# Performance work log

Measured on AMD Instinct MI355X. Metric: run time of the kernel, lower is better.

Reference implementation:

```python
import jax, jax.numpy as jnp
import numpy as np

B, S = 4, 2048          # batch, seq tokens
D_IN, D_HID = 1280, 2048  # from CAMERAMOE emb_size / d_inner
E, K = 8, 2             # num_experts, top_k
LN_EPS = 1e-6


def setup_inputs() -> dict:
    key = jax.random.key(0)
    ks = jax.random.split(key, 8)
    rn = lambda k, shp, sc=1.0: jax.random.normal(k, shp, dtype=jnp.float32) * sc
    return {
        "x": rn(ks[0], (B, S, D_IN)),
        "noise": rn(ks[1], (B, S, E)),          # the randn_like draw, made explicit
        "wr": rn(ks[2], (D_IN, E), 0.02), "br": jnp.zeros((E,), jnp.float32),
        "wn": rn(ks[3], (D_IN, E), 0.02), "bn": jnp.zeros((E,), jnp.float32),
        "w1": rn(ks[4], (E, D_IN, D_HID), 0.02), "b1": jnp.zeros((E, D_HID), jnp.float32),
        "w2": rn(ks[5], (E, D_HID, D_IN), 0.02), "b2": jnp.zeros((E, D_IN), jnp.float32),
        "gamma": jnp.ones((E, D_IN), jnp.float32), "beta": jnp.zeros((E, D_IN), jnp.float32),
    }


def reference(x, noise, wr, br, wn, bn, w1, b1, w2, b2, gamma, beta):
    # --- NoisyTopkRouter ---
    logits = x @ wr + br                                  # [B,S,E]
    noise_logits = x @ wn + bn                            # [B,S,E]
    noisy = logits + noise * jax.nn.softplus(noise_logits)
    _, idx = jax.lax.top_k(noisy, K)                      # [B,S,K]
    sel = jax.nn.one_hot(idx, E, dtype=bool).any(axis=-2) # [B,S,E] selected-expert mask
    sparse_logits = jnp.where(sel, noisy, -jnp.inf)       # scatter of top-k logits into -inf
    gates = jax.nn.softmax(sparse_logits, axis=-1)        # zeros for non-selected experts

    # --- SparseMoE combine (gate-weighted sum over experts; gate==0 masks out
    # non-selected tokens, matching the torch masked gather/scatter-add math) ---
    h = jax.nn.relu(jnp.einsum('bsd,edh->ebsh', x, w1) + b1[:, None, None, :])
    y = jnp.einsum('ebsh,ehd->ebsd', h, w2) + b2[:, None, None, :]
    y = y + x                                             # residual (broadcast over E)
    mu = y.mean(axis=-1, keepdims=True)
    var = y.var(axis=-1, keepdims=True)
    y = (y - mu) * jax.lax.rsqrt(var + LN_EPS)
    y = y * gamma[:, None, None, :] + beta[:, None, None, :]
    return jnp.einsum('ebsd,bse->bsd', y, gates)          # [B,S,D_IN]
```

## Files before the change

### kernel.cpp

```cpp
#include <hip/hip_runtime.h>
#include <stdint.h>

typedef unsigned short u16;
typedef __attribute__((ext_vector_type(8))) short short8;
typedef __attribute__((ext_vector_type(4))) float f32x4;
typedef __attribute__((ext_vector_type(4))) float float4v;
typedef __attribute__((ext_vector_type(4))) unsigned short us4;
typedef __attribute__((ext_vector_type(8))) unsigned short us8;

#define TOK   8192
#define DIN   1280
#define DHID  2048
#define NEXP  8
#define RCAP  17408
#define MT128 136

#define TRBLK1 5120
#define TRBLK2 5120
#define GABLKS 2048

__device__ __forceinline__ float bf2f(u16 u) {
  union { unsigned int i; float f; } v; v.i = ((unsigned int)u) << 16; return v.f;
}
__device__ __forceinline__ u16 f2bf(float f) {
  union { float f; unsigned int i; } v; v.f = f;
  unsigned int x = v.i;
  return (u16)((x + 0x7fffu + ((x >> 16) & 1u)) >> 16);
}

__device__ __forceinline__ void gload16(const u16* g, void* lds) {
  __builtin_amdgcn_global_load_lds(
      (const __attribute__((address_space(1))) unsigned int*)g,
      (__attribute__((address_space(3))) unsigned int*)lds, 16, 0, 0);
}

__global__ __launch_bounds__(256) void router_k(
    const float* __restrict__ x, const float* __restrict__ noise,
    const float* __restrict__ wr, const float* __restrict__ br,
    const float* __restrict__ wn, const float* __restrict__ bn,
    int* __restrict__ topk_e, float* __restrict__ topk_g)
{
  int w = threadIdx.x >> 6, lane = threadIdx.x & 63;
  int t0 = blockIdx.x * 8 + w * 2;
  int h = lane & 1, dl = lane >> 1;
  const float* xA = x + (size_t)t0 * DIN;
  const float* xB = xA + DIN;

  float ra[4], na[4], rb2[4], nb2[4];
  #pragma unroll
  for (int j = 0; j < 4; j++) { ra[j] = 0.f; na[j] = 0.f; rb2[j] = 0.f; nb2[j] = 0.f; }

  #pragma unroll 4
  for (int d0 = 0; d0 < DIN; d0 += 32) {
    int d = d0 + dl;
    float4v wrv = *(const float4v*)(wr + (size_t)d * 8 + h * 4);
    float4v wnv = *(const float4v*)(wn + (size_t)d * 8 + h * 4);
    float xa = xA[d], xb = xB[d];
    #pragma unroll
    for (int j = 0; j < 4; j++) {
      ra[j]  += xa * wrv[j]; na[j]  += xa * wnv[j];
      rb2[j] += xb * wrv[j]; nb2[j] += xb * wnv[j];
    }
  }
  #pragma unroll
  for (int off = 2; off < 64; off <<= 1) {
    #pragma unroll
    for (int j = 0; j < 4; j++) {
      ra[j]  += __shfl_xor(ra[j],  off);
      na[j]  += __shfl_xor(na[j],  off);
      rb2[j] += __shfl_xor(rb2[j], off);
      nb2[j] += __shfl_xor(nb2[j], off);
    }
  }
  float raO[4], naO[4], rbO[4], nbO[4];
  #pragma unroll
  for (int j = 0; j < 4; j++) {
    raO[j] = __shfl_xor(ra[j], 1);
    naO[j] = __shfl_xor(na[j], 1);
    rbO[j] = __shfl_xor(rb2[j], 1);
    nbO[j] = __shfl_xor(nb2[j], 1);
  }
  if (lane == 0) {
    #pragma unroll
    for (int tt = 0; tt < 2; tt++) {
      int t = t0 + tt;
      float noisy[8];
      #pragma unroll
      for (int j = 0; j < 4; j++) {
        float lg0 = (tt ? rb2[j] : ra[j]) + br[j];
        float nl0 = (tt ? nb2[j] : na[j]) + bn[j];
        float lg1 = (tt ? rbO[j] : raO[j]) + br[4 + j];
        float nl1 = (tt ? nbO[j] : naO[j]) + bn[4 + j];
        float sp0 = (nl0 > 0.f) ? nl0 + log1pf(expf(-nl0)) : log1pf(expf(nl0));
        float sp1 = (nl1 > 0.f) ? nl1 + log1pf(expf(-nl1)) : log1pf(expf(nl1));
        noisy[j]     = lg0 + noise[(size_t)t * 8 + j] * sp0;
        noisy[4 + j] = lg1 + noise[(size_t)t * 8 + 4 + j] * sp1;
      }
      int e0 = 0; float v0 = noisy[0];
      #pragma unroll
      for (int e = 1; e < 8; e++) if (noisy[e] > v0) { v0 = noisy[e]; e0 = e; }
      int e1 = -1; float v1 = -1e30f;
      #pragma unroll
      for (int e = 0; e < 8; e++) if (e != e0 && noisy[e] > v1) { v1 = noisy[e]; e1 = e; }
      float g0 = 1.f / (1.f + expf(v1 - v0));
      topk_e[2*t] = e0; topk_e[2*t+1] = e1;
      topk_g[2*t] = g0; topk_g[2*t+1] = 1.f - g0;
    }
  }
}

__global__ __launch_bounds__(1024) void scan_k(
    const int* __restrict__ topk_e, int* __restrict__ rowmap, int* __restrict__ aoffs)
{
  __shared__ int cnt[1024][8];
  __shared__ int tot[8];
  __shared__ int base[8];
  int tid = threadIdx.x;
  int ebuf[16];
  #pragma unroll
  for (int j = 0; j < 16; j++) ebuf[j] = topk_e[tid * 16 + j];
  int c0=0,c1=0,c2=0,c3=0,c4=0,c5=0,c6=0,c7=0;
  #pragma unroll
  for (int j = 0; j < 16; j++) {
    int e = ebuf[j];
    c0 += (e==0); c1 += (e==1); c2 += (e==2); c3 += (e==3);
    c4 += (e==4); c5 += (e==5); c6 += (e==6); c7 += (e==7);
  }
  cnt[tid][0]=c0; cnt[tid][1]=c1; cnt[tid][2]=c2; cnt[tid][3]=c3;
  cnt[tid][4]=c4; cnt[tid][5]=c5; cnt[tid][6]=c6; cnt[tid][7]=c7;
  __syncthreads();

  int w = tid >> 6, lane = tid & 63;
  if (w < 8) {
    int e = w;
    int s[16]; int run = 0;
    #pragma unroll
    for (int j = 0; j < 16; j++) { s[j] = run; run += cnt[lane*16+j][e]; }
    int inc = run;
    for (int off = 1; off < 64; off <<= 1) {
      int v = __shfl_up(inc, off);
      if (lane >= off) inc += v;
    }
    int lane_excl = inc - run;
    #pragma unroll
    for (int j = 0; j < 16; j++) cnt[lane*16+j][e] = lane_excl + s[j];
    if (lane == 63) tot[e] = inc;
  }
  __syncthreads();
  if (tid == 0) {
    int a = 0;
    for (int e = 0; e < 8; e++) { base[e] = a; aoffs[e] = a; a += (tot[e] + 127) & ~127; }
    aoffs[8] = a;
  }
  __syncthreads();
  int o0 = base[0]+cnt[tid][0], o1 = base[1]+cnt[tid][1], o2 = base[2]+cnt[tid][2],
      o3 = base[3]+cnt[tid][3], o4 = base[4]+cnt[tid][4], o5 = base[5]+cnt[tid][5],
      o6 = base[6]+cnt[tid][6], o7 = base[7]+cnt[tid][7];
  #pragma unroll
  for (int j = 0; j < 16; j++) {
    int e = ebuf[j];
    int row = o0;
    row = (e==1) ? o1 : row; row = (e==2) ? o2 : row; row = (e==3) ? o3 : row;
    row = (e==4) ? o4 : row; row = (e==5) ? o5 : row; row = (e==6) ? o6 : row;
    row = (e==7) ? o7 : row;
    o0 += (e==0); o1 += (e==1); o2 += (e==2); o3 += (e==3);
    o4 += (e==4); o5 += (e==5); o6 += (e==6); o7 += (e==7);
    rowmap[tid * 16 + j] = row;
  }
}

__global__ __launch_bounds__(256) void trga_k(
    const float* __restrict__ w1, u16* __restrict__ W1t,
    const float* __restrict__ w2, u16* __restrict__ W2t,
    const float* __restrict__ x, const int* __restrict__ rowmap,
    u16* __restrict__ Xe)
{
  __shared__ u16 ldsT[64 * 72];
  int id = blockIdx.x;
  int tid = threadIdx.x;
  int w = tid >> 6, lane = tid & 63;

  if (id < TRBLK1 + TRBLK2) {
    const float* in; u16* outp; int RK, CN, rb, cb;
    if (id < TRBLK1) {
      int e = id / 640, r = id % 640;
      RK = DIN; CN = DHID;
      rb = (r >> 5) * 64; cb = (r & 31) * 64;
      in = w1 + (size_t)e * RK * CN; outp = W1t + (size_t)e * RK * CN;
    } else {
      int id2 = id - TRBLK1;
      int e = id2 / 640, r = id2 % 640;
      RK = DHID; CN = DIN;
      rb = (r / 20) * 64; cb = (r % 20) * 64;
      in = w2 + (size_t)e * RK * CN; outp = W2t + (size_t)e * RK * CN;
    }
    {
      const float* src = in + (size_t)(rb + lane) * CN + cb + w * 16;
      u16 val[16];
      #pragma unroll
      for (int k = 0; k < 4; k++) {
        float4v v = *(const float4v*)(src + k * 4);
        #pragma unroll
        for (int j = 0; j < 4; j++) val[k * 4 + j] = f2bf(v[j]);
      }
      #pragma unroll
      for (int j = 0; j < 16; j++)
        ldsT[(w * 16 + j) * 72 + lane] = val[j];
    }
    __syncthreads();
    {
      int oc = tid >> 2, rch = (tid & 3) * 16;
      const u16* s = &ldsT[oc * 72 + rch];
      u16* d = outp + (size_t)(cb + oc) * RK + rb + rch;
      *(us8*)(d)     = *(const us8*)(s);
      *(us8*)(d + 8) = *(const us8*)(s + 8);
    }
    return;
  }

  int t = (id - (TRBLK1 + TRBLK2)) * 4 + w;
  int r0 = rowmap[2*t], r1 = rowmap[2*t+1];
  const float4v* xs = (const float4v*)(x + (size_t)t * DIN);
  us4* d0 = (us4*)(Xe + (size_t)r0 * DIN);
  us4* d1 = (us4*)(Xe + (size_t)r1 * DIN);
  #pragma unroll
  for (int i = 0; i < DIN / 4 / 64; i++) {
    int q = i * 64 + lane;
    float4v v = xs[q];
    us4 o;
    #pragma unroll
    for (int j = 0; j < 4; j++) o[j] = f2bf(v[j]);
    d0[q] = o;
    d1[q] = o;
  }
}

__global__ __launch_bounds__(256, 4) void gemm128_k(
    const u16* __restrict__ A, const u16* __restrict__ Bt,
    const float* __restrict__ bias, u16* __restrict__ Out,
    const int* __restrict__ aoffs, int K, int N, int relu)
{
  extern __shared__ u16 sm[];

  int nwgx = gridDim.x;
  int id = blockIdx.y * nwgx + blockIdx.x;
  int per = (nwgx * gridDim.y) >> 3;
  int sid = (id & 7) * per + (id >> 3);
  int bx = sid % nwgx, by = sid / nwgx;

  int row0 = by * 128;
  if (row0 >= aoffs[NEXP]) return;
  int e = 0;
  #pragma unroll
  for (int i = 0; i < NEXP; i++) if (row0 >= aoffs[i + 1]) e = i + 1;
  int ncol0 = bx * 128;
  const u16* Ab = A + (size_t)row0 * K;
  const u16* Bb = Bt + ((size_t)e * N + ncol0) * K;

  int tid = threadIdx.x, w = tid >> 6, lane = tid & 63;
  int wr = w >> 1, wc = w & 1;
  int l15 = lane & 15, l4 = lane >> 4;
  int xsw = (l15 >> 1) & 3;

  int srow[2], skc[2];
  #pragma unroll
  for (int q = 0; q < 2; q++) {
    int cd = q * 256 + tid;
    int cs = cd ^ ((cd >> 3) & 3);
    srow[q] = cs >> 2;
    skc[q]  = (cs & 3) * 8;
  }
  int ldsw = w * 1024;

  f32x4 acc[4][4];
  #pragma unroll
  for (int m = 0; m < 4; m++)
    #pragma unroll
    for (int n = 0; n < 4; n++) acc[m][n] = (f32x4){0.f, 0.f, 0.f, 0.f};

  short8 a[4], b[4];

#define STAGE_A(T, BUF) do {                                                  \
    char* d_ = (char*)sm + (BUF) * 16384;                                     \
    int ko_ = (T) * 32;                                                       \
    _Pragma("unroll")                                                         \
    for (int q = 0; q < 2; q++)                                               \
      gload16(Ab + (size_t)srow[q] * K + ko_ + skc[q], d_ + q*4096 + ldsw);   \
  } while (0)
#define STAGE_B(T, BUF) do {                                                  \
    char* d_ = (char*)sm + (BUF) * 16384 + 8192;                              \
    int ko_ = (T) * 32;                                                       \
    _Pragma("unroll")                                                         \
    for (int q = 0; q < 2; q++)                                               \
      gload16(Bb + (size_t)srow[q] * K + ko_ + skc[q], d_ + q*4096 + ldsw);   \
  } while (0)
#define RD_A() do {                                                           \
    _Pragma("unroll")                                                         \
    for (int m = 0; m < 4; m++) {                                             \
      int r_ = wr*64 + m*16 + l15;                                            \
      a[m] = *(const short8*)&smA[r_*32 + ((l4 ^ xsw) * 8)];                  \
    }                                                                         \
  } while (0)
#define RD_B() do {                                                           \
    _Pragma("unroll")                                                         \
    for (int n = 0; n < 4; n++) {                                             \
      int r_ = wc*64 + n*16 + l15;                                            \
      b[n] = *(const short8*)&smB[r_*32 + ((l4 ^ xsw) * 8)];                  \
    }                                                                         \
  } while (0)
#define MFMA16() do {                                                         \
    _Pragma("unroll")                                                         \
    for (int m = 0; m < 4; m++)                                               \
      _Pragma("unroll")                                                       \
      for (int n = 0; n < 4; n++)                                             \
        acc[m][n] = __builtin_amdgcn_mfma_f32_16x16x32_bf16(                  \
            a[m], b[n], acc[m][n], 0, 0, 0);                                  \
  } while (0)
#define BAR __builtin_amdgcn_s_barrier()

  int NT = K >> 5;
  STAGE_A(0, 0);
  STAGE_B(0, 0);
  STAGE_A(1, 1);
  STAGE_B(1, 1);
  asm volatile("s_waitcnt vmcnt(4)" ::: "memory");
  BAR;

  for (int t = 0; t < NT; ++t) {
    int buf = t & 1;
    const u16* smA = sm + buf * 8192;
    const u16* smB = smA + 4096;
    RD_A();
    RD_B();
    asm volatile("s_waitcnt lgkmcnt(0)" ::: "memory");
    BAR;
    if (t + 2 < NT) {
      STAGE_A(t + 2, buf);
      STAGE_B(t + 2, buf);
    }
    __builtin_amdgcn_s_setprio(1);
    MFMA16();
    __builtin_amdgcn_s_setprio(0);
    if (t + 2 < NT) {
      asm volatile("s_waitcnt vmcnt(4)" ::: "memory");
    } else if (t + 1 < NT) {
      asm volatile("s_waitcnt vmcnt(0)" ::: "memory");
    }
    BAR;
  }
#undef STAGE_A
#undef STAGE_B
#undef RD_A
#undef RD_B
#undef MFMA16
#undef BAR

  #pragma unroll
  for (int in = 0; in < 4; in++) {
    int c = ncol0 + wc * 64 + in * 16 + l15;
    float bv = bias[(size_t)e * N + c];
    #pragma unroll
    for (int im = 0; im < 4; im++) {
      int rb = row0 + wr * 64 + im * 16 + l4 * 4;
      #pragma unroll
      for (int j = 0; j < 4; j++) {
        float v = acc[im][in][j] + bv;
        if (relu) v = fmaxf(v, 0.f);
        Out[(size_t)(rb + j) * N + c] = f2bf(v);
      }
    }
  }
}

__global__ __launch_bounds__(256) void ln_k(
    const float* __restrict__ x, const u16* __restrict__ Y,
    const int* __restrict__ rowmap, const int* __restrict__ topk_e,
    const float* __restrict__ topk_g, const float* __restrict__ gamma,
    const float* __restrict__ beta, float* __restrict__ out)
{
  int w = threadIdx.x >> 6, lane = threadIdx.x & 63;
  int t = blockIdx.x * 4 + w;
  int r0 = rowmap[2*t], r1 = rowmap[2*t+1];
  int e0 = topk_e[2*t], e1 = topk_e[2*t+1];
  float g0 = topk_g[2*t], g1 = topk_g[2*t+1];
  const float4v* xt = (const float4v*)(x + (size_t)t * DIN);
  const us4* y0p = (const us4*)(Y + (size_t)r0 * DIN);
  const us4* y1p = (const us4*)(Y + (size_t)r1 * DIN);
  float4v v0[5], v1[5];
  float s0 = 0.f, q0 = 0.f, s1 = 0.f, q1 = 0.f;
  #pragma unroll
  for (int i = 0; i < 5; i++) {
    int q = i * 64 + lane;
    float4v xv = xt[q];
    us4 ya = y0p[q], yb = y1p[q];
    #pragma unroll
    for (int j = 0; j < 4; j++) {
      float aa = xv[j] + bf2f(ya[j]);
      float bb = xv[j] + bf2f(yb[j]);
      v0[i][j] = aa; v1[i][j] = bb;
      s0 += aa; q0 += aa * aa; s1 += bb; q1 += bb * bb;
    }
  }
  #pragma unroll
  for (int off = 32; off; off >>= 1) {
    s0 += __shfl_xor(s0, off); q0 += __shfl_xor(q0, off);
    s1 += __shfl_xor(s1, off); q1 += __shfl_xor(q1, off);
  }
  const float inv = 1.f / DIN;
  float mu0 = s0 * inv, mu1 = s1 * inv;
  float rs0 = rsqrtf(fmaxf(q0 * inv - mu0 * mu0, 0.f) + 1e-6f);
  float rs1 = rsqrtf(fmaxf(q1 * inv - mu1 * mu1, 0.f) + 1e-6f);
  const float4v* ga0 = (const float4v*)(gamma + (size_t)e0 * DIN);
  const float4v* be0 = (const float4v*)(beta  + (size_t)e0 * DIN);
  const float4v* ga1 = (const float4v*)(gamma + (size_t)e1 * DIN);
  const float4v* be1 = (const float4v*)(beta  + (size_t)e1 * DIN);
  float4v* op = (float4v*)(out + (size_t)t * DIN);
  #pragma unroll
  for (int i = 0; i < 5; i++) {
    int q = i * 64 + lane;
    float4v gA = ga0[q], bA = be0[q], gB = ga1[q], bB = be1[q];
    float4v o;
    #pragma unroll
    for (int j = 0; j < 4; j++) {
      float n0 = (v0[i][j] - mu0) * rs0 * gA[j] + bA[j];
      float n1 = (v1[i][j] - mu1) * rs1 * gB[j] + bB[j];
      o[j] = g0 * n0 + g1 * n1;
    }
    op[q] = o;
  }
}

extern "C" void kernel_launch(void* const* d_in, const int* in_sizes, int n_in,
                              void* d_out, int out_size, void* d_ws, size_t ws_size,
                              hipStream_t stream)
{
  const float* x     = (const float*)d_in[0];
  const float* noise = (const float*)d_in[1];
  const float* wr    = (const float*)d_in[2];
  const float* br    = (const float*)d_in[3];
  const float* wn    = (const float*)d_in[4];
  const float* bn    = (const float*)d_in[5];
  const float* w1    = (const float*)d_in[6];
  const float* b1    = (const float*)d_in[7];
  const float* w2    = (const float*)d_in[8];
  const float* b2    = (const float*)d_in[9];
  const float* gamma = (const float*)d_in[10];
  const float* beta  = (const float*)d_in[11];
  float* out = (float*)d_out;
  char* ws = (char*)d_ws;

  int*   aoffs   = (int*)(ws + 128);
  int*   rowmap  = (int*)(ws + 4096);
  int*   topk_e  = (int*)(ws + 4096 + 65536);
  float* topk_g  = (float*)(ws + 4096 + 2 * 65536);

  const size_t XE_OFF   = (size_t)1 << 20;
  const size_t XE_BYTES = (size_t)RCAP * DIN * 2;
  const size_t H_BYTES  = (size_t)RCAP * DHID * 2;
  const size_t WT_BYTES = (size_t)NEXP * DHID * DIN * 2;
  u16* Xe  = (u16*)(ws + XE_OFF);
  u16* Hb  = (u16*)(ws + XE_OFF + XE_BYTES);
  u16* Yb  = Xe;
  u16* W1t = (u16*)(ws + XE_OFF + XE_BYTES + H_BYTES);
  u16* W2t = (u16*)(ws + XE_OFF + XE_BYTES + H_BYTES + WT_BYTES);

  router_k<<<TOK/8, 256, 0, stream>>>(x, noise, wr, br, wn, bn, topk_e, topk_g);
  scan_k<<<1, 1024, 0, stream>>>(topk_e, rowmap, aoffs);
  trga_k<<<TRBLK1 + TRBLK2 + GABLKS, 256, 0, stream>>>(w1, W1t, w2, W2t, x, rowmap, Xe);
  gemm128_k<<<dim3(DHID/128, MT128), 256, 32768, stream>>>(Xe, W1t, b1, Hb, aoffs, DIN, DHID, 1);
  gemm128_k<<<dim3(DIN/128, MT128), 256, 32768, stream>>>(Hb, W2t, b2, Yb, aoffs, DHID, DIN, 0);
  ln_k<<<TOK/4, 256, 0, stream>>>(x, Yb, rowmap, topk_e, topk_g, gamma, beta, out);
}
```

Measured before the change: 376.4 us.

## Add 256x256 8-wave ping-pong GEMM for W1 and widen K-tile to 64

The first expert GEMM now runs a new 256x256-tile kernel with 512 threads and 128KB of LDS. It interleaves half-tile loads with MFMA phases, and per-expert row padding grows to 256. The second GEMM keeps 128x128 tiles but moves to a K-step of 64, with an 8-way XOR LDS swizzle and 64KB of shared memory. The aim is more data reuse per tile and fewer barriers per FLOP. The cost is more padding rows, lower occupancy and heavier register pressure.

After: 366.4 us. -2.7%, faster.

```diff
diff --git a/kernel.cpp b/kernel.cpp
--- a/kernel.cpp
+++ b/kernel.cpp
@@ -12,8 +12,9 @@
 #define DIN   1280
 #define DHID  2048
 #define NEXP  8
-#define RCAP  17408
-#define MT128 136
+#define RCAP  18432
+#define MT128 144
+#define MT256 72
 
 #define TRBLK1 5120
 #define TRBLK2 5120
@@ -149,7 +150,7 @@
   __syncthreads();
   if (tid == 0) {
     int a = 0;
-    for (int e = 0; e < 8; e++) { base[e] = a; aoffs[e] = a; a += (tot[e] + 127) & ~127; }
+    for (int e = 0; e < 8; e++) { base[e] = a; aoffs[e] = a; a += (tot[e] + 255) & ~255; }
     aoffs[8] = a;
   }
   __syncthreads();
@@ -235,7 +236,7 @@
   }
 }
 
-__global__ __launch_bounds__(256, 4) void gemm128_k(
+__global__ __launch_bounds__(512, 2) void gemm256p8_k(
     const u16* __restrict__ A, const u16* __restrict__ Bt,
     const float* __restrict__ bias, u16* __restrict__ Out,
     const int* __restrict__ aoffs, int K, int N, int relu)
@@ -248,6 +249,177 @@
   int sid = (id & 7) * per + (id >> 3);
   int bx = sid % nwgx, by = sid / nwgx;
 
+  int row0 = by * 256;
+  if (row0 >= aoffs[NEXP]) return;
+  int e = 0;
+  #pragma unroll
+  for (int i = 0; i < NEXP; i++) if (row0 >= aoffs[i + 1]) e = i + 1;
+  int ncol0 = bx * 256;
+  const u16* Ab = A + (size_t)row0 * K;
+  const u16* Bb = Bt + ((size_t)e * N + ncol0) * K;
+
+  int tid = threadIdx.x, w = tid >> 6, lane = tid & 63;
+  int wr = w >> 2, wcn = w & 3;
+  int l15 = lane & 15, l4 = lane >> 4;
+  int xorv = (l15 & 7) << 3;
+
+  int srow[2], skc[2];
+  #pragma unroll
+  for (int q = 0; q < 2; q++) {
+    int cd = q * 512 + tid;
+    int cs = cd ^ ((cd >> 3) & 7);
+    srow[q] = cs >> 3;
+    skc[q]  = (cs & 7) * 8;
+  }
+  int ldsw = w * 1024;
+
+  f32x4 acc[8][4];
+  #pragma unroll
+  for (int m = 0; m < 8; m++)
+    #pragma unroll
+    for (int n = 0; n < 4; n++) acc[m][n] = (f32x4){0.f, 0.f, 0.f, 0.f};
+
+  short8 a[4][2], b0[2][2], b1[2][2];
+
+#define STAGE_AH(T, BUF, HF) do {                                             \
+    char* d_ = (char*)sm + ((BUF)*2 + (HF)) * 16384;                          \
+    _Pragma("unroll")                                                         \
+    for (int q = 0; q < 2; q++)                                               \
+      gload16(Ab + (size_t)((HF)*128 + srow[q]) * K + (T)*64 + skc[q],        \
+              d_ + q*8192 + ldsw);                                            \
+  } while (0)
+#define STAGE_BH(T, BUF, HF) do {                                             \
+    char* d_ = (char*)sm + 65536 + ((BUF)*2 + (HF)) * 16384;                  \
+    _Pragma("unroll")                                                         \
+    for (int q = 0; q < 2; q++)                                               \
+      gload16(Bb + (size_t)((HF)*128 + srow[q]) * K + (T)*64 + skc[q],        \
+              d_ + q*8192 + ldsw);                                            \
+  } while (0)
+#define RDA(BUF, MH) do {                                                     \
+    const u16* s_ = sm + ((BUF)*2 + wr) * 8192;                               \
+    _Pragma("unroll")                                                         \
+    for (int m = 0; m < 4; m++)                                               \
+      _Pragma("unroll")                                                       \
+      for (int ks = 0; ks < 2; ks++) {                                        \
+        int r_ = (MH)*64 + m*16 + l15;                                        \
+        a[m][ks] = *(const short8*)&s_[(r_*64 + (ks*4 + l4)*8) ^ xorv];       \
+      }                                                                       \
+  } while (0)
+#define RDB(BUF, DST, NH) do {                                                \
+    const u16* s_ = sm + 32768 + ((BUF)*2 + (wcn >> 1)) * 8192;               \
+    _Pragma("unroll")                                                         \
+    for (int n = 0; n < 2; n++)                                               \
+      _Pragma("unroll")                                                       \
+      for (int ks = 0; ks < 2; ks++) {                                        \
+        int r_ = (wcn & 1)*64 + (NH)*32 + n*16 + l15;                         \
+        DST[n][ks] = *(const short8*)&s_[(r_*64 + (ks*4 + l4)*8) ^ xorv];     \
+      }                                                                       \
+  } while (0)
+#define M16(MH, NH, BB) do {                                                  \
+    __builtin_amdgcn_s_setprio(1);                                            \
+    _Pragma("unroll")                                                         \
+    for (int m = 0; m < 4; m++)                                               \
+      _Pragma("unroll")                                                       \
+      for (int n = 0; n < 2; n++)                                             \
+        _Pragma("unroll")                                                     \
+        for (int ks = 0; ks < 2; ks++)                                        \
+          acc[(MH)*4+m][(NH)*2+n] = __builtin_amdgcn_mfma_f32_16x16x32_bf16(  \
+              a[m][ks], BB[n][ks], acc[(MH)*4+m][(NH)*2+n], 0, 0, 0);         \
+    __builtin_amdgcn_s_setprio(0);                                            \
+  } while (0)
+#define BAR __builtin_amdgcn_s_barrier()
+#define LGKM0 asm volatile("s_waitcnt lgkmcnt(0)" ::: "memory")
+
+  int NT = K >> 6;
+  STAGE_AH(0, 0, 0); STAGE_AH(0, 0, 1);
+  STAGE_BH(0, 0, 0); STAGE_BH(0, 0, 1);
+  STAGE_BH(1, 1, 0); STAGE_BH(1, 1, 1);
+  asm volatile("s_waitcnt vmcnt(4)" ::: "memory");
+  BAR;
+
+  for (int i = 0; i < (NT >> 1); ++i) {
+    int T0 = 2*i, T1 = 2*i + 1;
+    RDA(0, 0); RDB(0, b0, 0);
+    STAGE_AH(T1, 1, 0);
+    BAR; LGKM0;
+    M16(0, 0, b0);
+    BAR;
+    RDB(0, b1, 1);
+    STAGE_AH(T1, 1, 1);
+    BAR; LGKM0;
+    M16(0, 1, b1);
+    BAR;
+    RDA(0, 1);
+    if (T0 + 2 < NT) STAGE_BH(T0 + 2, 0, 0);
+    BAR; LGKM0;
+    M16(1, 1, b1);
+    BAR;
+    if (T0 + 2 < NT) STAGE_BH(T0 + 2, 0, 1);
+    BAR;
+    M16(1, 0, b0);
+    if (T0 + 2 < NT) { asm volatile("s_waitcnt vmcnt(4)" ::: "memory"); }
+    else             { asm volatile("s_waitcnt vmcnt(0)" ::: "memory"); }
+    BAR;
+    RDA(1, 0); RDB(1, b0, 0);
+    if (T0 + 2 < NT) STAGE_AH(T0 + 2, 0, 0);
+    BAR; LGKM0;
+    M16(0, 0, b0);
+    BAR;
+    RDB(1, b1, 1);
+    if (T0 + 2 < NT) STAGE_AH(T0 + 2, 0, 1);
+    BAR; LGKM0;
+    M16(0, 1, b1);
+    BAR;
+    RDA(1, 1);
+    if (T1 + 2 < NT) STAGE_BH(T1 + 2, 1, 0);
+    BAR; LGKM0;
+    M16(1, 1, b1);
+    BAR;
+    if (T1 + 2 < NT) STAGE_BH(T1 + 2, 1, 1);
+    BAR;
+    M16(1, 0, b0);
+    if (T1 + 2 < NT) { asm volatile("s_waitcnt vmcnt(4)" ::: "memory"); }
+    else             { asm volatile("s_waitcnt vmcnt(0)" ::: "memory"); }
+    BAR;
+  }
+#undef STAGE_AH
+#undef STAGE_BH
+#undef RDA
+#undef RDB
+#undef M16
+#undef BAR
+#undef LGKM0
+
+  #pragma unroll
+  for (int ni = 0; ni < 4; ni++) {
+    int c = ncol0 + wcn * 64 + ni * 16 + l15;
+    float bv = bias[(size_t)e * N + c];
+    #pragma unroll
+    for (int mi = 0; mi < 8; mi++) {
+      int rb = row0 + wr * 128 + mi * 16 + l4 * 4;
+      #pragma unroll
+      for (int j = 0; j < 4; j++) {
+        float v = acc[mi][ni][j] + bv;
+        if (relu) v = fmaxf(v, 0.f);
+        Out[(size_t)(rb + j) * N + c] = f2bf(v);
+      }
+    }
+  }
+}
+
+__global__ __launch_bounds__(256, 2) void gemm128_k(
+    const u16* __restrict__ A, const u16* __restrict__ Bt,
+    const float* __restrict__ bias, u16* __restrict__ Out,
+    const int* __restrict__ aoffs, int K, int N, int relu)
+{
+  extern __shared__ u16 sm[];
+
+  int nwgx = gridDim.x;
+  int id = blockIdx.y * nwgx + blockIdx.x;
+  int per = (nwgx * gridDim.y) >> 3;
+  int sid = (id & 7) * per + (id >> 3);
+  int bx = sid % nwgx, by = sid / nwgx;
+
   int row0 = by * 128;
   if (row0 >= aoffs[NEXP]) return;
   int e = 0;
@@ -260,15 +432,15 @@
   int tid = threadIdx.x, w = tid >> 6, lane = tid & 63;
   int wr = w >> 1, wc = w & 1;
   int l15 = lane & 15, l4 = lane >> 4;
-  int xsw = (l15 >> 1) & 3;
-
-  int srow[2], skc[2];
-  #pragma unroll
-  for (int q = 0; q < 2; q++) {
+  int xorv = (l15 & 7) << 3;
+
+  int srow[4], skc[4];
+  #pragma unroll
+  for (int q = 0; q < 4; q++) {
     int cd = q * 256 + tid;
-    int cs = cd ^ ((cd >> 3) & 3);
-    srow[q] = cs >> 2;
-    skc[q]  = (cs & 3) * 8;
+    int cs = cd ^ ((cd >> 3) & 7);
+    srow[q] = cs >> 3;
+    skc[q]  = (cs & 7) * 8;
   }
   int ldsw = w * 1024;
 
@@ -278,60 +450,67 @@
     #pragma unroll
     for (int n = 0; n < 4; n++) acc[m][n] = (f32x4){0.f, 0.f, 0.f, 0.f};
 
-  short8 a[4], b[4];
+  short8 a[4][2], b0[2][2], b1[2][2];
 
 #define STAGE_A(T, BUF) do {                                                  \
-    char* d_ = (char*)sm + (BUF) * 16384;                                     \
-    int ko_ = (T) * 32;                                                       \
-    _Pragma("unroll")                                                         \
-    for (int q = 0; q < 2; q++)                                               \
+    char* d_ = (char*)sm + (BUF) * 32768;                                     \
+    int ko_ = (T) * 64;                                                       \
+    _Pragma("unroll")                                                         \
+    for (int q = 0; q < 4; q++)                                               \
       gload16(Ab + (size_t)srow[q] * K + ko_ + skc[q], d_ + q*4096 + ldsw);   \
   } while (0)
 #define STAGE_B(T, BUF) do {                                                  \
-    char* d_ = (char*)sm + (BUF) * 16384 + 8192;                              \
-    int ko_ = (T) * 32;                                                       \
-    _Pragma("unroll")                                                         \
-    for (int q = 0; q < 2; q++)                                               \
+    char* d_ = (char*)sm + (BUF) * 32768 + 16384;                             \
+    int ko_ = (T) * 64;                                                       \
+    _Pragma("unroll")                                                         \
+    for (int q = 0; q < 4; q++)                                               \
       gload16(Bb + (size_t)srow[q] * K + ko_ + skc[q], d_ + q*4096 + ldsw);   \
   } while (0)
 #define RD_A() do {                                                           \
-    _Pragma("unroll")                                                         \
-    for (int m = 0; m < 4; m++) {                                             \
-      int r_ = wr*64 + m*16 + l15;                                            \
-      a[m] = *(const short8*)&smA[r_*32 + ((l4 ^ xsw) * 8)];                  \
-    }                                                                         \
-  } while (0)
-#define RD_B() do {                                                           \
-    _Pragma("unroll")                                                         \
-    for (int n = 0; n < 4; n++) {                                             \
-      int r_ = wc*64 + n*16 + l15;                                            \
-      b[n] = *(const short8*)&smB[r_*32 + ((l4 ^ xsw) * 8)];                  \
-    }                                                                         \
-  } while (0)
-#define MFMA16() do {                                                         \
     _Pragma("unroll")                                                         \
     for (int m = 0; m < 4; m++)                                               \
       _Pragma("unroll")                                                       \
-      for (int n = 0; n < 4; n++)                                             \
-        acc[m][n] = __builtin_amdgcn_mfma_f32_16x16x32_bf16(                  \
-            a[m], b[n], acc[m][n], 0, 0, 0);                                  \
+      for (int ks = 0; ks < 2; ks++) {                                        \
+        int r_ = wr*64 + m*16 + l15;                                          \
+        a[m][ks] = *(const short8*)&smA[(r_*64 + ks*32 + l4*8) ^ xorv];       \
+      }                                                                       \
+  } while (0)
+#define RD_B(DST, NH) do {                                                    \
+    _Pragma("unroll")                                                         \
+    for (int n = 0; n < 2; n++)                                               \
+      _Pragma("unroll")                                                       \
+      for (int ks = 0; ks < 2; ks++) {                                        \
+        int r_ = wc*64 + (NH)*32 + n*16 + l15;                                \
+        DST[n][ks] = *(const short8*)&smB[(r_*64 + ks*32 + l4*8) ^ xorv];     \
+      }                                                                       \
+  } while (0)
+#define MFMA16(NH, BB) do {                                                   \
+    _Pragma("unroll")                                                         \
+    for (int m = 0; m < 4; m++)                                               \
+      _Pragma("unroll")                                                       \
+      for (int n = 0; n < 2; n++)                                             \
+        _Pragma("unroll")                                                     \
+        for (int ks = 0; ks < 2; ks++)                                        \
+          acc[m][(NH)*2+n] = __builtin_amdgcn_mfma_f32_16x16x32_bf16(         \
+              a[m][ks], BB[n][ks], acc[m][(NH)*2+n], 0, 0, 0);                \
   } while (0)
 #define BAR __builtin_amdgcn_s_barrier()
 
-  int NT = K >> 5;
+  int NT = K >> 6;
   STAGE_A(0, 0);
   STAGE_B(0, 0);
   STAGE_A(1, 1);
   STAGE_B(1, 1);
-  asm volatile("s_waitcnt vmcnt(4)" ::: "memory");
+  asm volatile("s_waitcnt vmcnt(8)" ::: "memory");
   BAR;
 
   for (int t = 0; t < NT; ++t) {
     int buf = t & 1;
-    const u16* smA = sm + buf * 8192;
-    const u16* smB = smA + 4096;
+    const u16* smA = sm + buf * 16384;
+    const u16* smB = smA + 8192;
     RD_A();
-    RD_B();
+    RD_B(b0, 0);
+    RD_B(b1, 1);
     asm volatile("s_waitcnt lgkmcnt(0)" ::: "memory");
     BAR;
     if (t + 2 < NT) {
@@ -339,10 +518,11 @@
       STAGE_B(t + 2, buf);
     }
     __builtin_amdgcn_s_setprio(1);
-    MFMA16();
+    MFMA16(0, b0);
+    MFMA16(1, b1);
     __builtin_amdgcn_s_setprio(0);
     if (t + 2 < NT) {
-      asm volatile("s_waitcnt vmcnt(4)" ::: "memory");
+      asm volatile("s_waitcnt vmcnt(8)" ::: "memory");
     } else if (t + 1 < NT) {
       asm volatile("s_waitcnt vmcnt(0)" ::: "memory");
     }
@@ -467,7 +647,7 @@
   router_k<<<TOK/8, 256, 0, stream>>>(x, noise, wr, br, wn, bn, topk_e, topk_g);
   scan_k<<<1, 1024, 0, stream>>>(topk_e, rowmap, aoffs);
   trga_k<<<TRBLK1 + TRBLK2 + GABLKS, 256, 0, stream>>>(w1, W1t, w2, W2t, x, rowmap, Xe);
-  gemm128_k<<<dim3(DHID/128, MT128), 256, 32768, stream>>>(Xe, W1t, b1, Hb, aoffs, DIN, DHID, 1);
-  gemm128_k<<<dim3(DIN/128, MT128), 256, 32768, stream>>>(Hb, W2t, b2, Yb, aoffs, DHID, DIN, 0);
+  gemm256p8_k<<<dim3(DHID/256, MT256), 512, 131072, stream>>>(Xe, W1t, b1, Hb, aoffs, DIN, DHID, 1);
+  gemm128_k<<<dim3(DIN/128, MT128), 256, 65536, stream>>>(Hb, W2t, b2, Yb, aoffs, DHID, DIN, 0);
   ln_k<<<TOK/4, 256, 0, stream>>>(x, Yb, rowmap, topk_e, topk_g, gamma, beta, out);
 }
```
